# Optimization experiments

Measured on AMD Instinct MI355X. Metric: run time of the kernel, lower is better.

Reference implementation:

```python
import jax, jax.numpy as jnp
import numpy as np

EMBED = 1024
HEADS = 16
HEAD_DIM = EMBED // HEADS
NEG = -1e20


def setup_inputs() -> dict:
    key = jax.random.key(0)
    ks = jax.random.split(key, 12)
    N, S, E = 2, 2048, EMBED
    w = lambda k: (jax.random.normal(k, (E, E), dtype=jnp.float32) * 0.02)
    b = lambda k: (jax.random.normal(k, (E,), dtype=jnp.float32) * 0.02)
    return {
        "values": jax.random.normal(ks[0], (N, S, E), dtype=jnp.float32),
        "keys": jax.random.normal(ks[1], (N, S, E), dtype=jnp.float32),
        "query": jax.random.normal(ks[2], (N, S, E), dtype=jnp.float32),
        "mask": jnp.ones((N, S), dtype=jnp.int32),
        "Wv": w(ks[3]), "bv": b(ks[4]),
        "Wk": w(ks[5]), "bk": b(ks[6]),
        "Wq": w(ks[7]), "bq": b(ks[8]),
        "Wo": w(ks[9]), "bo": b(ks[10]),
    }


def reference(values, keys, query, mask, Wv, bv, Wk, bk, Wq, bq, Wo, bo):
    N, S, E = query.shape
    # torch nn.Linear: x @ W.T + b
    v = (values @ Wv.T + bv).reshape(N, S, HEADS, HEAD_DIM)
    k = (keys @ Wk.T + bk).reshape(N, S, HEADS, HEAD_DIM)
    q = (query @ Wq.T + bq).reshape(N, S, HEADS, HEAD_DIM)
    # full [N,H,Q,K] score matrix, as in the original einsum
    energy = jnp.einsum('nqhd,nkhd->nhqk', q, k)
    # 2D mask with mismatched dims triggers causal tril path in the original
    causal = jnp.tril(jnp.ones((S, S), dtype=bool))  # [Q,K]
    energy = jnp.where(causal[None, None, :, :], energy, NEG)
    # NOTE: original scales by sqrt(embed_size), not sqrt(head_dim)
    attn = jax.nn.softmax(energy / jnp.sqrt(jnp.float32(E)), axis=3)
    out = jnp.einsum('nhqk,nkhd->nqhd', attn, v).reshape(N, S, E)
    return out @ Wo.T + bo
```

## Files before the change

### kernel.cpp

```cpp
#include <hip/hip_runtime.h>

typedef __bf16 bf16;
typedef __bf16 bf16x4 __attribute__((ext_vector_type(4)));
typedef __bf16 bf16x8 __attribute__((ext_vector_type(8)));
typedef float floatx4 __attribute__((ext_vector_type(4)));

#define GLOAD_LDS16(gp, lp) \
  __builtin_amdgcn_global_load_lds( \
      (const __attribute__((address_space(1))) void*)(gp), \
      (__attribute__((address_space(3))) void*)(lp), 16, 0, 0)

__global__ __launch_bounds__(256) void cvt_all_kernel(
    const float* __restrict__ v, const float* __restrict__ k, const float* __restrict__ q,
    const float* __restrict__ wv, const float* __restrict__ wk,
    const float* __restrict__ wq, const float* __restrict__ wo,
    bf16* __restrict__ xv, bf16* __restrict__ xk, bf16* __restrict__ xq,
    bf16* __restrict__ bwv, bf16* __restrict__ bwk, bf16* __restrict__ bwq,
    bf16* __restrict__ bwo) {
  const int i = blockIdx.x * 256 + threadIdx.x;
  const int A4 = 1 << 20;
  const float* src; bf16* dst; int off;
  if (i < A4)            { src = v; dst = xv; off = i; }
  else if (i < 2 * A4)   { src = k; dst = xk; off = i - A4; }
  else if (i < 3 * A4)   { src = q; dst = xq; off = i - 2 * A4; }
  else {
    int j = i - 3 * A4; int r = j >> 18; off = j & ((1 << 18) - 1);
    src = (r == 0) ? wv : (r == 1) ? wk : (r == 2) ? wq : wo;
    dst = (r == 0) ? bwv : (r == 1) ? bwk : (r == 2) ? bwq : bwo;
  }
  float4 x = reinterpret_cast<const float4*>(src)[off];
  union { bf16 b[4]; short4 s; } u;
  u.b[0] = (bf16)x.x; u.b[1] = (bf16)x.y; u.b[2] = (bf16)x.z; u.b[3] = (bf16)x.w;
  reinterpret_cast<short4*>(dst)[off] = u.s;
}

template <int MODE>
__device__ __forceinline__ void gemm_body(
    const bf16* __restrict__ A, const bf16* __restrict__ B,
    const float* __restrict__ bias, void* __restrict__ Cout) {
  constexpr int K = 1024, N = 1024;
  __shared__ __align__(16) bf16 As[128 * 32];
  __shared__ __align__(16) bf16 Bs[128 * 32];
  const int tid = threadIdx.x;
  const int lane = tid & 63;
  const int wave = tid >> 6;
  const int quad = lane >> 4;
  const int l16 = lane & 15;
  const int wm = (wave >> 1) * 64;
  const int wn = (wave & 1) * 64;
  const int am0 = blockIdx.y * 128;
  const int bn0 = blockIdx.x * 128;
  const int srow = lane >> 2;
  const int scol = (lane & 3) * 8;

  floatx4 acc[4][4] = {};

  for (int k0 = 0; k0 < K; k0 += 32) {
    __syncthreads();
#pragma unroll
    for (int j = 0; j < 2; j++) {
      const int chunk = wave * 2 + j;
      const int row = chunk * 16 + srow;
      GLOAD_LDS16(A + (size_t)(am0 + row) * K + k0 + scol, As + chunk * 512);
      GLOAD_LDS16(B + (size_t)(bn0 + row) * K + k0 + scol, Bs + chunk * 512);
    }
    __syncthreads();

    bf16x8 af[4], bfv[4];
#pragma unroll
    for (int mi = 0; mi < 4; mi++)
      af[mi] = *reinterpret_cast<const bf16x8*>(&As[(wm + mi * 16 + l16) * 32 + quad * 8]);
#pragma unroll
    for (int ni = 0; ni < 4; ni++)
      bfv[ni] = *reinterpret_cast<const bf16x8*>(&Bs[(wn + ni * 16 + l16) * 32 + quad * 8]);
#pragma unroll
    for (int mi = 0; mi < 4; mi++)
#pragma unroll
      for (int ni = 0; ni < 4; ni++)
        acc[mi][ni] = __builtin_amdgcn_mfma_f32_16x16x32_bf16(af[mi], bfv[ni], acc[mi][ni], 0, 0, 0);
  }

#pragma unroll
  for (int mi = 0; mi < 4; mi++) {
#pragma unroll
    for (int ni = 0; ni < 4; ni++) {
      const int col = bn0 + wn + ni * 16 + l16;
      const float bb = bias[col];
      const int row = am0 + wm + mi * 16 + quad * 4;
      if constexpr (MODE == 2) {
#pragma unroll
        for (int r = 0; r < 4; r++)
          reinterpret_cast<float*>(Cout)[(size_t)(row + r) * N + col] = acc[mi][ni][r] + bb;
      } else {
        const int nb = row >> 11;
        const int s = row & 2047;
        const int h = col >> 6;
        const int d = col & 63;
        const int nh = nb * 16 + h;
        if constexpr (MODE == 0) {
          bf16* base = reinterpret_cast<bf16*>(Cout) + ((size_t)nh * 2048 + s) * 64 + d;
#pragma unroll
          for (int r = 0; r < 4; r++) base[(size_t)r * 64] = (bf16)(acc[mi][ni][r] + bb);
        } else {
          bf16x4 pk;
#pragma unroll
          for (int r = 0; r < 4; r++) pk[r] = (bf16)(acc[mi][ni][r] + bb);
          *reinterpret_cast<bf16x4*>(
              reinterpret_cast<bf16*>(Cout) + ((size_t)nh * 64 + d) * 2048 + s) = pk;
        }
      }
    }
  }
}

__global__ __launch_bounds__(256) void gemm_qkv(
    const bf16* __restrict__ A0, const bf16* __restrict__ B0, const float* __restrict__ c0, bf16* __restrict__ C0,
    const bf16* __restrict__ A1, const bf16* __restrict__ B1, const float* __restrict__ c1, bf16* __restrict__ C1,
    const bf16* __restrict__ A2, const bf16* __restrict__ B2, const float* __restrict__ c2, bf16* __restrict__ C2) {
  if (blockIdx.z == 0)      gemm_body<0>(A0, B0, c0, C0);
  else if (blockIdx.z == 1) gemm_body<0>(A1, B1, c1, C1);
  else                      gemm_body<1>(A2, B2, c2, C2);
}

__global__ __launch_bounds__(256) void gemm_out(
    const bf16* __restrict__ A, const bf16* __restrict__ B,
    const float* __restrict__ bias, float* __restrict__ C) {
  gemm_body<2>(A, B, bias, C);
}

#define S_LEN 2048
#define EMB 1024
#define QT 128
#define KTILE 64
#define PSTR 72
#define SCALE2 (0.03125f * 1.44269504f)

__global__ __launch_bounds__(256) void attn_kernel(
    const bf16* __restrict__ Qh, const bf16* __restrict__ Kh,
    const bf16* __restrict__ Vt, bf16* __restrict__ O) {
  __shared__ __align__(16) bf16 Ks[KTILE * 64];
  __shared__ __align__(16) bf16 Vs[64 * KTILE];
  __shared__ __align__(16) bf16 Ps[QT * PSTR];

  const int tid = threadIdx.x;
  const int lane = tid & 63;
  const int wave = tid >> 6;
  const int quad = lane >> 4;
  const int l16 = lane & 15;
  const int wq = wave * 32;

  const int id = blockIdx.x;
  const int p = id & 255;
  const int half = id >> 8;
  const int qtl = p & 7;
  const int qt = half ? (15 - qtl) : qtl;
  const int nh = p >> 3;
  const int n = nh >> 4;
  const int h = nh & 15;
  const int q0 = qt * QT;

  bf16x8 aq[2][2];
  {
    const bf16* Qb = Qh + ((size_t)nh * S_LEN + q0 + wq + l16) * 64 + quad * 8;
#pragma unroll
    for (int mi = 0; mi < 2; mi++)
#pragma unroll
      for (int kc = 0; kc < 2; kc++)
        aq[mi][kc] = *reinterpret_cast<const bf16x8*>(Qb + mi * 16 * 64 + kc * 32);
  }

  float l_part[2][4] = {};
  floatx4 o_acc[2][4] = {};

  const bf16* Kbase = Kh + (size_t)nh * S_LEN * 64;
  const bf16* Vbase = Vt + (size_t)nh * 64 * S_LEN;

  const int srl = lane >> 3;
  const int sc8 = lane & 7;

  const int ktiles = 2 * qt + 2;
  for (int kt = 0; kt < ktiles; kt++) {
    const int k0 = kt * KTILE;

    __syncthreads();
#pragma unroll
    for (int j = 0; j < 2; j++) {
      const int rl = wave * 16 + j * 8 + srl;
      const int c8 = ((sc8 ^ (rl & 7)) * 8);
      GLOAD_LDS16(Kbase + (size_t)(k0 + rl) * 64 + c8, Ks + (wave * 16 + j * 8) * 64);
      GLOAD_LDS16(Vbase + (size_t)rl * S_LEN + k0 + c8, Vs + (wave * 16 + j * 8) * 64);
    }
    __syncthreads();

    floatx4 s_acc[2][4] = {};
#pragma unroll
    for (int kc = 0; kc < 2; kc++) {
      bf16x8 bk[4];
#pragma unroll
      for (int ni = 0; ni < 4; ni++)
        bk[ni] = *reinterpret_cast<const bf16x8*>(
            &Ks[(ni * 16 + l16) * 64 + (((kc * 4 + quad) ^ (l16 & 7)) * 8)]);
#pragma unroll
      for (int mi = 0; mi < 2; mi++)
#pragma unroll
        for (int ni = 0; ni < 4; ni++)
          s_acc[mi][ni] = __builtin_amdgcn_mfma_f32_16x16x32_bf16(aq[mi][kc], bk[ni], s_acc[mi][ni], 0, 0, 0);
    }

    const bool needMask = (k0 + KTILE - 1) > (q0 + wq);
#pragma unroll
    for (int mi = 0; mi < 2; mi++) {
#pragma unroll
      for (int ni = 0; ni < 4; ni++) {
        const int cg = k0 + ni * 16 + l16;
#pragma unroll
        for (int r = 0; r < 4; r++) {
          const int rg = q0 + wq + mi * 16 + quad * 4 + r;
          float pr = __builtin_amdgcn_exp2f(s_acc[mi][ni][r] * SCALE2);
          if (needMask) pr = (cg <= rg) ? pr : 0.f;
          s_acc[mi][ni][r] = pr;
          l_part[mi][r] += pr;
        }
      }
    }

#pragma unroll
    for (int mi = 0; mi < 2; mi++) {
#pragma unroll
      for (int ni = 0; ni < 4; ni++) {
        const int cl = ni * 2 + (l16 >> 3);
        const int pc = (cl ^ quad) * 8 + (l16 & 7);
#pragma unroll
        for (int r = 0; r < 4; r++)
          Ps[(wq + mi * 16 + quad * 4 + r) * PSTR + pc] = (bf16)s_acc[mi][ni][r];
      }
    }

#pragma unroll
    for (int kc = 0; kc < 2; kc++) {
      bf16x8 ap[2], bv[4];
      const int pc = ((kc * 4 + quad) ^ (l16 >> 2)) * 8;
#pragma unroll
      for (int mi = 0; mi < 2; mi++)
        ap[mi] = *reinterpret_cast<const bf16x8*>(&Ps[(wq + mi * 16 + l16) * PSTR + pc]);
#pragma unroll
      for (int di = 0; di < 4; di++)
        bv[di] = *reinterpret_cast<const bf16x8*>(
            &Vs[(di * 16 + l16) * 64 + (((kc * 4 + quad) ^ (l16 & 7)) * 8)]);
#pragma unroll
      for (int mi = 0; mi < 2; mi++)
#pragma unroll
        for (int di = 0; di < 4; di++)
          o_acc[mi][di] = __builtin_amdgcn_mfma_f32_16x16x32_bf16(ap[mi], bv[di], o_acc[mi][di], 0, 0, 0);
    }
  }

#pragma unroll
  for (int mi = 0; mi < 2; mi++)
#pragma unroll
    for (int r = 0; r < 4; r++) {
      float s = l_part[mi][r];
#pragma unroll
      for (int off = 1; off < 16; off <<= 1) s += __shfl_xor(s, off);
      l_part[mi][r] = 1.0f / s;
    }

  bf16* Op = O + ((size_t)(n * S_LEN + q0 + wq)) * EMB + h * 64;
#pragma unroll
  for (int mi = 0; mi < 2; mi++) {
#pragma unroll
    for (int r = 0; r < 4; r++) {
      const float inv = l_part[mi][r];
      bf16* orow = Op + (size_t)(mi * 16 + quad * 4 + r) * EMB;
#pragma unroll
      for (int di = 0; di < 4; di++)
        orow[di * 16 + l16] = (bf16)(o_acc[mi][di][r] * inv);
    }
  }
}

extern "C" void kernel_launch(void* const* d_in, const int* in_sizes, int n_in,
                              void* d_out, int out_size, void* d_ws, size_t ws_size,
                              hipStream_t stream) {
  (void)in_sizes; (void)n_in; (void)out_size; (void)ws_size;
  const float* values = (const float*)d_in[0];
  const float* keys   = (const float*)d_in[1];
  const float* query  = (const float*)d_in[2];
  const float* Wv = (const float*)d_in[4];
  const float* bv = (const float*)d_in[5];
  const float* Wk = (const float*)d_in[6];
  const float* bk = (const float*)d_in[7];
  const float* Wq = (const float*)d_in[8];
  const float* bq = (const float*)d_in[9];
  const float* Wo = (const float*)d_in[10];
  const float* bo = (const float*)d_in[11];
  float* out = (float*)d_out;

  const int NB = 2, S = 2048, E = 1024;
  const int M = NB * S;
  const size_t MB_ = 1u << 20;
  char* ws = (char*)d_ws;
  bf16* xv  = (bf16*)(ws + 0 * MB_);
  bf16* xk  = (bf16*)(ws + 8 * MB_);
  bf16* xq  = (bf16*)(ws + 16 * MB_);
  bf16* wvb = (bf16*)(ws + 24 * MB_);
  bf16* wkb = (bf16*)(ws + 26 * MB_);
  bf16* wqb = (bf16*)(ws + 28 * MB_);
  bf16* wob = (bf16*)(ws + 30 * MB_);
  bf16* kh  = (bf16*)(ws + 32 * MB_);
  bf16* qh  = (bf16*)(ws + 40 * MB_);
  bf16* vt  = (bf16*)(ws + 48 * MB_);
  bf16* ao  = (bf16*)(ws + 56 * MB_);

  cvt_all_kernel<<<(4 << 20) / 256, 256, 0, stream>>>(
      values, keys, query, Wv, Wk, Wq, Wo,
      xv, xk, xq, wvb, wkb, wqb, wob);

  gemm_qkv<<<dim3(E / 128, M / 128, 3), 256, 0, stream>>>(
      xq, wqb, bq, qh,
      xk, wkb, bk, kh,
      xv, wvb, bv, vt);

  attn_kernel<<<dim3(512), 256, 0, stream>>>(qh, kh, vt, ao);

  gemm_out<<<dim3(E / 128, M / 128), 256, 0, stream>>>(ao, wob, bo, out);
}
```

Measured before the change: 239.6 us.

## Split long causal attention tiles across two blocks and stage QKV epilogue through LDS

The attention grid becomes 256x3. Short query tiles run whole, and each long query tile's key range is split between two blocks. Those two blocks write unnormalized fp32 partial outputs and row sums to workspace, and a new combine kernel merges and normalizes them. This evens out the per-block load of the causal triangle. Separately, the QKV GEMM epilogue now transposes results through swizzled shared memory so it can issue 16-byte coalesced stores for both the head-major and transposed-V layouts. The cost is an extra kernel launch plus fp32 partial traffic.

```diff
diff --git a/kernel.cpp b/kernel.cpp
--- a/kernel.cpp
+++ b/kernel.cpp
@@ -39,8 +39,9 @@
     const bf16* __restrict__ A, const bf16* __restrict__ B,
     const float* __restrict__ bias, void* __restrict__ Cout) {
   constexpr int K = 1024, N = 1024;
-  __shared__ __align__(16) bf16 As[128 * 32];
-  __shared__ __align__(16) bf16 Bs[128 * 32];
+  __shared__ __align__(16) bf16 SMEM[8192];
+  bf16* As = SMEM;
+  bf16* Bs = SMEM + 4096;
   const int tid = threadIdx.x;
   const int lane = tid & 63;
   const int wave = tid >> 6;
@@ -80,33 +81,78 @@
         acc[mi][ni] = __builtin_amdgcn_mfma_f32_16x16x32_bf16(af[mi], bfv[ni], acc[mi][ni], 0, 0, 0);
   }
 
-#pragma unroll
-  for (int mi = 0; mi < 4; mi++) {
-#pragma unroll
-    for (int ni = 0; ni < 4; ni++) {
-      const int col = bn0 + wn + ni * 16 + l16;
-      const float bb = bias[col];
-      const int row = am0 + wm + mi * 16 + quad * 4;
-      if constexpr (MODE == 2) {
+  if constexpr (MODE == 2) {
+#pragma unroll
+    for (int mi = 0; mi < 4; mi++) {
+#pragma unroll
+      for (int ni = 0; ni < 4; ni++) {
+        const int col = bn0 + wn + ni * 16 + l16;
+        const float bb = bias[col];
+        const int row = am0 + wm + mi * 16 + quad * 4;
 #pragma unroll
         for (int r = 0; r < 4; r++)
           reinterpret_cast<float*>(Cout)[(size_t)(row + r) * N + col] = acc[mi][ni][r] + bb;
-      } else {
-        const int nb = row >> 11;
-        const int s = row & 2047;
-        const int h = col >> 6;
-        const int d = col & 63;
-        const int nh = nb * 16 + h;
-        if constexpr (MODE == 0) {
-          bf16* base = reinterpret_cast<bf16*>(Cout) + ((size_t)nh * 2048 + s) * 64 + d;
-#pragma unroll
-          for (int r = 0; r < 4; r++) base[(size_t)r * 64] = (bf16)(acc[mi][ni][r] + bb);
-        } else {
-          bf16x4 pk;
-#pragma unroll
-          for (int r = 0; r < 4; r++) pk[r] = (bf16)(acc[mi][ni][r] + bb);
-          *reinterpret_cast<bf16x4*>(
-              reinterpret_cast<bf16*>(Cout) + ((size_t)nh * 64 + d) * 2048 + s) = pk;
+      }
+    }
+  } else {
+    __syncthreads();
+    bf16* T = SMEM + wave * 2048;
+    const int nb = (am0 + wm) >> 11;
+    const int sq0 = (am0 + wm) & 2047;
+    const int h = (bn0 + wn) >> 6;
+    const int nh = nb * 16 + h;
+    const int r8 = lane >> 3, c8 = lane & 7;
+
+    if constexpr (MODE == 0) {
+#pragma unroll
+      for (int pp = 0; pp < 2; pp++) {
+#pragma unroll
+        for (int mm = 0; mm < 2; mm++) {
+          const int mi = pp * 2 + mm;
+#pragma unroll
+          for (int ni = 0; ni < 4; ni++) {
+            const int d = ni * 16 + l16;
+            const float bc = bias[bn0 + wn + d];
+#pragma unroll
+            for (int r = 0; r < 4; r++) {
+              const int s = mm * 16 + quad * 4 + r;
+              T[s * 64 + (d & 7) + 8 * ((d >> 3) ^ (s & 7))] = (bf16)(acc[mi][ni][r] + bc);
+            }
+          }
+        }
+#pragma unroll
+        for (int it = 0; it < 4; it++) {
+          const int s = it * 8 + r8;
+          bf16x8 vv = *reinterpret_cast<const bf16x8*>(&T[s * 64 + ((c8 ^ r8) * 8)]);
+          *reinterpret_cast<bf16x8*>(
+              reinterpret_cast<bf16*>(Cout) +
+              ((size_t)nh * 2048 + sq0 + pp * 32 + s) * 64 + c8 * 8) = vv;
+        }
+      }
+    } else {
+#pragma unroll
+      for (int pp = 0; pp < 2; pp++) {
+#pragma unroll
+        for (int nn = 0; nn < 2; nn++) {
+          const int ni = pp * 2 + nn;
+          const int dp = nn * 16 + l16;
+          const float bc = bias[bn0 + wn + pp * 32 + dp];
+#pragma unroll
+          for (int mi = 0; mi < 4; mi++) {
+#pragma unroll
+            for (int r = 0; r < 4; r++) {
+              const int s = mi * 16 + quad * 4 + r;
+              T[dp * 64 + (s & 7) + 8 * ((s >> 3) ^ (dp & 7))] = (bf16)(acc[mi][ni][r] + bc);
+            }
+          }
+        }
+#pragma unroll
+        for (int it = 0; it < 4; it++) {
+          const int dp = it * 8 + r8;
+          bf16x8 vv = *reinterpret_cast<const bf16x8*>(&T[dp * 64 + ((c8 ^ r8) * 8)]);
+          *reinterpret_cast<bf16x8*>(
+              reinterpret_cast<bf16*>(Cout) +
+              ((size_t)nh * 64 + pp * 32 + dp) * 2048 + sq0 + c8 * 8) = vv;
         }
       }
     }
@@ -137,7 +183,8 @@
 
 __global__ __launch_bounds__(256) void attn_kernel(
     const bf16* __restrict__ Qh, const bf16* __restrict__ Kh,
-    const bf16* __restrict__ Vt, bf16* __restrict__ O) {
+    const bf16* __restrict__ Vt, bf16* __restrict__ O,
+    float* __restrict__ Opart, float* __restrict__ lpart) {
   __shared__ __align__(16) bf16 Ks[KTILE * 64];
   __shared__ __align__(16) bf16 Vs[64 * KTILE];
   __shared__ __align__(16) bf16 Ps[QT * PSTR];
@@ -149,14 +196,20 @@
   const int l16 = lane & 15;
   const int wq = wave * 32;
 
-  const int id = blockIdx.x;
-  const int p = id & 255;
-  const int half = id >> 8;
-  const int qtl = p & 7;
-  const int qt = half ? (15 - qtl) : qtl;
-  const int nh = p >> 3;
+  const int c = blockIdx.x;
+  const int role = blockIdx.y;
+  const int nh = c >> 3;
+  const int t = c & 7;
   const int n = nh >> 4;
   const int h = nh & 15;
+  int qt, kt0, kt1;
+  if (role == 0) { qt = t; kt0 = 0; kt1 = 2 * t + 2; }
+  else {
+    qt = 15 - t;
+    const int halfk = qt + 1;
+    kt0 = (role == 1) ? 0 : halfk;
+    kt1 = (role == 1) ? halfk : 2 * halfk;
+  }
   const int q0 = qt * QT;
 
   bf16x8 aq[2][2];
@@ -178,17 +231,16 @@
   const int srl = lane >> 3;
   const int sc8 = lane & 7;
 
-  const int ktiles = 2 * qt + 2;
-  for (int kt = 0; kt < ktiles; kt++) {
+  for (int kt = kt0; kt < kt1; kt++) {
     const int k0 = kt * KTILE;
 
     __syncthreads();
 #pragma unroll
     for (int j = 0; j < 2; j++) {
       const int rl = wave * 16 + j * 8 + srl;
-      const int c8 = ((sc8 ^ (rl & 7)) * 8);
-      GLOAD_LDS16(Kbase + (size_t)(k0 + rl) * 64 + c8, Ks + (wave * 16 + j * 8) * 64);
-      GLOAD_LDS16(Vbase + (size_t)rl * S_LEN + k0 + c8, Vs + (wave * 16 + j * 8) * 64);
+      const int c8s = ((sc8 ^ (rl & 7)) * 8);
+      GLOAD_LDS16(Kbase + (size_t)(k0 + rl) * 64 + c8s, Ks + (wave * 16 + j * 8) * 64);
+      GLOAD_LDS16(Vbase + (size_t)rl * S_LEN + k0 + c8s, Vs + (wave * 16 + j * 8) * 64);
     }
     __syncthreads();
 
@@ -262,20 +314,68 @@
       float s = l_part[mi][r];
 #pragma unroll
       for (int off = 1; off < 16; off <<= 1) s += __shfl_xor(s, off);
-      l_part[mi][r] = 1.0f / s;
-    }
-
-  bf16* Op = O + ((size_t)(n * S_LEN + q0 + wq)) * EMB + h * 64;
-#pragma unroll
-  for (int mi = 0; mi < 2; mi++) {
-#pragma unroll
-    for (int r = 0; r < 4; r++) {
-      const float inv = l_part[mi][r];
-      bf16* orow = Op + (size_t)(mi * 16 + quad * 4 + r) * EMB;
-#pragma unroll
-      for (int di = 0; di < 4; di++)
-        orow[di * 16 + l16] = (bf16)(o_acc[mi][di][r] * inv);
-    }
+      l_part[mi][r] = s;
+    }
+
+  if (role == 0) {
+    bf16* Op = O + ((size_t)(n * S_LEN + q0 + wq)) * EMB + h * 64;
+#pragma unroll
+    for (int mi = 0; mi < 2; mi++) {
+#pragma unroll
+      for (int r = 0; r < 4; r++) {
+        const float inv = 1.0f / l_part[mi][r];
+        bf16* orow = Op + (size_t)(mi * 16 + quad * 4 + r) * EMB;
+#pragma unroll
+        for (int di = 0; di < 4; di++)
+          orow[di * 16 + l16] = (bf16)(o_acc[mi][di][r] * inv);
+      }
+    }
+  } else {
+    float* Ob = Opart + ((size_t)c * 2 + (role - 1)) * (QT * 64);
+    float* lb = lpart + ((size_t)c * 2 + (role - 1)) * QT;
+#pragma unroll
+    for (int mi = 0; mi < 2; mi++)
+#pragma unroll
+      for (int r = 0; r < 4; r++)
+        if (l16 == 0) lb[wq + mi * 16 + quad * 4 + r] = l_part[mi][r];
+#pragma unroll
+    for (int mi = 0; mi < 2; mi++)
+#pragma unroll
+      for (int r = 0; r < 4; r++) {
+        float* orow = Ob + (size_t)(wq + mi * 16 + quad * 4 + r) * 64;
+#pragma unroll
+        for (int di = 0; di < 4; di++)
+          orow[di * 16 + l16] = o_acc[mi][di][r];
+      }
+  }
+}
+
+__global__ __launch_bounds__(256) void attn_combine(
+    const float* __restrict__ Opart, const float* __restrict__ lpart,
+    bf16* __restrict__ O) {
+  const int c = blockIdx.x;
+  const int nh = c >> 3;
+  const int t = c & 7;
+  const int qt = 15 - t;
+  const int n = nh >> 4;
+  const int h = nh & 15;
+  const float* O1 = Opart + (size_t)c * 2 * (QT * 64);
+  const float* O2 = O1 + QT * 64;
+  const float* l1 = lpart + (size_t)c * 2 * QT;
+  const float* l2 = l1 + QT;
+  const int tid = threadIdx.x;
+  for (int i = tid; i < QT * 64 / 4; i += 256) {
+    const int row = i >> 4;
+    const float inv = 1.0f / (l1[row] + l2[row]);
+    float4 a = reinterpret_cast<const float4*>(O1)[i];
+    float4 b = reinterpret_cast<const float4*>(O2)[i];
+    bf16x4 pk;
+    pk[0] = (bf16)((a.x + b.x) * inv);
+    pk[1] = (bf16)((a.y + b.y) * inv);
+    pk[2] = (bf16)((a.z + b.z) * inv);
+    pk[3] = (bf16)((a.w + b.w) * inv);
+    *reinterpret_cast<bf16x4*>(
+        O + ((size_t)(n * S_LEN + qt * QT + row)) * EMB + h * 64 + (i & 15) * 4) = pk;
   }
 }
 
@@ -311,6 +411,8 @@
   bf16* qh  = (bf16*)(ws + 40 * MB_);
   bf16* vt  = (bf16*)(ws + 48 * MB_);
   bf16* ao  = (bf16*)(ws + 56 * MB_);
+  float* Opart = (float*)(ws + 0 * MB_);
+  float* lpart = (float*)(ws + 17 * MB_);
 
   cvt_all_kernel<<<(4 << 20) / 256, 256, 0, stream>>>(
       values, keys, query, Wv, Wk, Wq, Wo,
@@ -321,7 +423,8 @@
       xk, wkb, bk, kh,
       xv, wvb, bv, vt);
 
-  attn_kernel<<<dim3(512), 256, 0, stream>>>(qh, kh, vt, ao);
+  attn_kernel<<<dim3(256, 3), 256, 0, stream>>>(qh, kh, vt, ao, Opart, lpart);
+  attn_combine<<<dim3(256), 256, 0, stream>>>(Opart, lpart, ao);
 
   gemm_out<<<dim3(E / 128, M / 128), 256, 0, stream>>>(ao, wob, bo, out);
 }
```

Measured after the change: 242.5 us. Within noise of the previous version (+1.2%).
